# Kernel tuning notes

Measured on AMD Instinct MI355X. Metric: run time of the kernel, lower is better.

Reference implementation:

```python
import jax, jax.numpy as jnp
import numpy as np

B, N, C = 512, 32, 1024


def setup_inputs() -> dict:
    key = jax.random.key(0)
    k1, k2, k3 = jax.random.split(key, 3)
    x = jax.random.normal(k1, (B, N, C), dtype=jnp.float32)
    # Conv1d(in=2, out=1, kernel_size=3): weight [O, I, W], bias [O]
    fan_in = 2 * 3
    bound = 1.0 / np.sqrt(fan_in)
    conv_w = jax.random.uniform(k2, (1, 2, 3), dtype=jnp.float32, minval=-bound, maxval=bound)
    conv_b = jax.random.uniform(k3, (1,), dtype=jnp.float32, minval=-bound, maxval=bound)
    return {"x": x, "conv_w": conv_w, "conv_b": conv_b}


def _merge_step(x, conv_w, conv_b):
    # x: [B, n, C] -> [B, n-1, C]
    b, n, c = x.shape
    # pairwise euclidean distances via gram matrix (avoids [B,n,n,C] blowup)
    sq = jnp.sum(x * x, axis=-1)  # [B, n]
    d2 = sq[:, :, None] + sq[:, None, :] - 2.0 * jnp.einsum('bic,bjc->bij', x, x)
    dist = jnp.sqrt(jnp.maximum(d2, 0.0))  # [B, n, n]
    # global max over ALL batches (as torch.max(all_dist)), then mask diagonal
    m = jnp.max(dist)
    di = jnp.arange(n)
    dist = dist.at[:, di, di].set(m + 1.0)
    # per-batch argmin over flattened matrix, unravel
    flat_idx = jnp.argmin(dist.reshape(b, -1), axis=1)
    a = flat_idx // n
    bb = flat_idx % n
    a, bb = jnp.minimum(a, bb), jnp.maximum(a, bb)  # ensure a < b
    # replicate the exact (buggy-faithful) index-list construction:
    # rows[a]=0; rows[0]=a; rows[b]=1; rows[1]=b  (sequential assignments)
    bi = jnp.arange(b)
    perm = jnp.broadcast_to(jnp.arange(n), (b, n))
    perm = perm.at[bi, a].set(0)
    perm = perm.at[bi, 0].set(a)
    perm = perm.at[bi, bb].set(1)
    perm = perm.at[bi, 1].set(bb)
    xg = jnp.take_along_axis(x, perm[:, :, None], axis=1)  # [B, n, C]
    to_merge = xg[:, 0:2, :]      # [B, 2, C]
    remaining = xg[:, 2:, :]      # [B, n-2, C]
    merged = jax.lax.conv_general_dilated(
        to_merge, conv_w, window_strides=(1,), padding='SAME',
        dimension_numbers=('NCH', 'OIH', 'NCH'))  # [B, 1, C]
    merged = jax.nn.relu(merged + conv_b[None, :, None])
    return jnp.concatenate([merged, remaining], axis=1)


def reference(x, conv_w, conv_b):
    b, n, c = x.shape
    for _ in range(n - 1):
        x = _merge_step(x, conv_w, conv_b)
    return x[:, 0, :]  # final squeeze: [B, C]
```

## Files before the change

kernel.cpp:

```cpp
#include <hip/hip_runtime.h>
#include <stdint.h>

#define BDIM    512
#define NROWS   32
#define CDIM    1024
#define NSTEPS  31
#define BATCH   512

__device__ __forceinline__ float reduce4f(float a0, float a1, float a2, float a3, int lane) {
    float t, r, b01, b23, c;
    t = (lane & 1) ? a0 : a1; r = (lane & 1) ? a1 : a0; b01 = r + __shfl_xor(t, 1);
    t = (lane & 1) ? a2 : a3; r = (lane & 1) ? a3 : a2; b23 = r + __shfl_xor(t, 1);
    t = (lane & 2) ? b01 : b23; r = (lane & 2) ? b23 : b01; c = r + __shfl_xor(t, 2);
    c += __shfl_xor(c, 4); c += __shfl_xor(c, 8); c += __shfl_xor(c, 16); c += __shfl_xor(c, 32);
    return c;
}

__global__ __launch_bounds__(BDIM, 4)
void merge_tree_kernel(const float* __restrict__ xin,
                       const float* __restrict__ wz,
                       const float* __restrict__ bz,
                       float* __restrict__ out)
{
    const int b    = blockIdx.x;
    const int tid  = threadIdx.x;
    const int lane = tid & 63;
    const int wid  = tid >> 6;

    const float* xb = xin + (size_t)b * NROWS * CDIM;

    __shared__ float  D[NROWS][NROWS + 1];
    __shared__ float4 mA4[4 * 64];
    __shared__ float4 mB4[4 * 64];
    __shared__ int    idxbuf[2][NROWS];
    __shared__ int    posb[NROWS];
    __shared__ int    bankSlot[32];
    __shared__ unsigned long long wp[8];

    const float w00 = wz[0], w01 = wz[1], w02 = wz[2];
    const float w10 = wz[3], w11 = wz[4], w12 = wz[5];
    const float cb  = bz[0];

    float R[4][16];
    float m[16];
    float nxt[16];

    if (tid < NROWS) {
        idxbuf[0][tid] = tid;
        posb[tid] = tid;
        bankSlot[tid] = (tid >> 2) + ((tid & 3) << 3);
    }

    {
        const float4* src = (const float4*)xb;
        #pragma unroll
        for (int q = 0; q < 4; q++) {
            float4 t = src[lane * 4 + q];
            m[4*q] = t.x; m[4*q+1] = t.y; m[4*q+2] = t.z; m[4*q+3] = t.w;
        }
    }
    #pragma unroll 1
    for (int i = 0; i < NROWS; i++) {
        if (i < NROWS - 1) {
            const float4* src = (const float4*)(xb + (size_t)(i + 1) * CDIM);
            #pragma unroll
            for (int q = 0; q < 4; q++) {
                float4 t = src[lane * 4 + q];
                nxt[4*q] = t.x; nxt[4*q+1] = t.y; nxt[4*q+2] = t.z; nxt[4*q+3] = t.w;
            }
        }
        float accv[4];
        #pragma unroll
        for (int k = 0; k < 4; k++) {
            const int s = wid + (k << 3);
            float acc0 = 0.0f, acc1 = 0.0f;
            if (s < i) {
                #pragma unroll
                for (int e = 0; e < 8; e++) {
                    float d0 = m[e] - R[k][e];
                    float d1 = m[e + 8] - R[k][e + 8];
                    acc0 += d0 * d0;
                    acc1 += d1 * d1;
                }
            } else if (s == i) {
                #pragma unroll
                for (int e = 0; e < 16; e++) R[k][e] = m[e];
            }
            accv[k] = acc0 + acc1;
        }
        float c = reduce4f(accv[0], accv[1], accv[2], accv[3], lane);
        int s_lane = wid + ((lane & 3) << 3);
        if (lane < 4 && s_lane < i) { D[i][s_lane] = c; D[s_lane][i] = c; }

        if (i < NROWS - 1) {
            #pragma unroll
            for (int e = 0; e < 16; e++) m[e] = nxt[e];
        }
    }
    __syncthreads();

    int p = 0;
    #pragma unroll 1
    for (int step = 0; step < NSTEPS; step++) {
        const int n = NROWS - step;
        int* idx  = idxbuf[p];
        int* nidx = idxbuf[p ^ 1];
        const uint32_t M = 0xFFFFFFFFu / (uint32_t)n + 1u;

        unsigned long long bk = ~0ull;
        #pragma unroll
        for (int r = 0; r < (NROWS * NROWS) / BDIM; r++) {
            const int flat = r * BDIM + tid;
            const int s = flat >> 5, t = flat & 31;
            const int li = posb[s], lj = posb[t];
            if (t > s && li < n && lj < n) {
                uint32_t d2b = __float_as_uint(D[s][t]);
                int i2 = (li < lj) ? li : lj;
                int j2 = (li < lj) ? lj : li;
                unsigned long long key =
                    ((unsigned long long)d2b << 10) | (unsigned)(i2 * n + j2);
                bk = (key < bk) ? key : bk;
            }
        }
        #pragma unroll
        for (int off = 1; off < 64; off <<= 1) {
            unsigned long long ov = __shfl_xor(bk, off);
            bk = (ov < bk) ? ov : bk;
        }
        if (lane == 0) wp[wid] = bk;
        __syncthreads();

        bk = wp[0];
        #pragma unroll
        for (int w = 1; w < 8; w++) {
            unsigned long long ov = wp[w];
            bk = (ov < bk) ? ov : bk;
        }
        const int bp  = (int)(bk & 1023u);
        const int a   = (int)__umulhi((uint32_t)bp, M);
        const int bbj = bp - a * n;
        const int sa  = idx[a], sb = idx[bbj];
        const int deadSlot = (a == 1) ? idx[0] : sa;

        #pragma unroll
        for (int k = 0; k < 4; k++) {
            const int s = bankSlot[wid * 4 + k];
            if (s == sa || s == sb) {
                float hl = __shfl_up(R[k][15], 1);  if (lane == 0)  hl = 0.0f;
                float hr = __shfl_down(R[k][0], 1); if (lane == 63) hr = 0.0f;
                float4* dst = (s == sa) ? mA4 : mB4;
                const float c0 = (s == sa) ? w00 : w10;
                const float c1 = (s == sa) ? w01 : w11;
                const float c2 = (s == sa) ? w02 : w12;
                #pragma unroll
                for (int q = 0; q < 4; q++) {
                    float vv[4];
                    #pragma unroll
                    for (int j = 0; j < 4; j++) {
                        const int e = 4 * q + j;
                        float xm1 = (e == 0)  ? hl : R[k][e - 1];
                        float xp1 = (e == 15) ? hr : R[k][e + 1];
                        vv[j] = c0 * xm1 + c1 * R[k][e] + c2 * xp1;
                    }
                    dst[q * 64 + lane] = make_float4(vv[0], vv[1], vv[2], vv[3]);
                }
            }
        }
        if (tid == 0) { nidx[0] = sb; posb[sb] = 0; posb[deadSlot] = 127; }
        if (tid >= 1 && tid < n - 1) {
            int kk = tid + 1;
            int src = (kk == bbj) ? 1 : ((kk == a) ? 0 : kk);
            int sl2 = idx[src];
            nidx[tid] = sl2;
            posb[sl2] = tid;
        }
        __syncthreads();

        #pragma unroll
        for (int q = 0; q < 4; q++) {
            float4 va = mA4[q * 64 + lane];
            float4 vb = mB4[q * 64 + lane];
            float v0 = cb + va.x + vb.x;
            float v1 = cb + va.y + vb.y;
            float v2 = cb + va.z + vb.z;
            float v3 = cb + va.w + vb.w;
            m[4*q+0] = v0 > 0.0f ? v0 : 0.0f;
            m[4*q+1] = v1 > 0.0f ? v1 : 0.0f;
            m[4*q+2] = v2 > 0.0f ? v2 : 0.0f;
            m[4*q+3] = v3 > 0.0f ? v3 : 0.0f;
        }
        float accv[4]; int slv[4];
        #pragma unroll
        for (int k = 0; k < 4; k++) {
            int s = bankSlot[wid * 4 + k];
            if (s == sb) {
                #pragma unroll
                for (int e = 0; e < 16; e++) R[k][e] = m[e];
            }
            if (s == deadSlot) {
                if (lane == 0) bankSlot[wid * 4 + k] = -1;
                s = -1;
            }
            const int live = (s >= 0 && s != sb) ? s : -1;
            slv[k] = live;
            float acc0 = 0.0f, acc1 = 0.0f;
            if (live >= 0) {
                #pragma unroll
                for (int e = 0; e < 8; e++) {
                    float d0 = m[e] - R[k][e];
                    float d1 = m[e + 8] - R[k][e + 8];
                    acc0 += d0 * d0;
                    acc1 += d1 * d1;
                }
            }
            accv[k] = acc0 + acc1;
        }
        float c = reduce4f(accv[0], accv[1], accv[2], accv[3], lane);
        int s_lane = slv[0];
        s_lane = ((lane & 3) == 1) ? slv[1] : s_lane;
        s_lane = ((lane & 3) == 2) ? slv[2] : s_lane;
        s_lane = ((lane & 3) == 3) ? slv[3] : s_lane;
        if (lane < 4 && s_lane >= 0) {
            D[sb][s_lane] = c; D[s_lane][sb] = c;
        }
        __syncthreads();
        p ^= 1;
    }

    if (wid == 0) {
        float4* od = (float4*)(out + (size_t)b * CDIM);
        #pragma unroll
        for (int q = 0; q < 4; q++)
            od[lane * 4 + q] = make_float4(m[4*q], m[4*q+1], m[4*q+2], m[4*q+3]);
    }
}

extern "C" void kernel_launch(void* const* d_in, const int* in_sizes, int n_in,
                              void* d_out, int out_size, void* d_ws, size_t ws_size,
                              hipStream_t stream) {
    const float* x  = (const float*)d_in[0];
    const float* w  = (const float*)d_in[1];
    const float* cb = (const float*)d_in[2];
    float* out = (float*)d_out;
    (void)d_ws; (void)ws_size; (void)in_sizes; (void)n_in; (void)out_size;

    hipLaunchKernelGGL(merge_tree_kernel, dim3(BATCH), dim3(BDIM), 0, stream,
                       x, w, cb, out);
}
```

Measured before the change: 214.0 us.

## Drop per-step barrier by double-buffering positions and folding new-row distances into argmin

Position lookups are double-buffered and computed directly from the previous permutation, so the per-thread index update no longer scatters into a shared array. The distances of the freshly merged row are reduced per wave into extra partial-min slots, and that row is excluded from the full-matrix scan. This removes the trailing __syncthreads of each merge step. It relies on the remaining barrier to order D writes and wp slot reuse, and on the position encoding (flat index = new position of the partner row, assuming the merged row sits at position 0), which is subtle and could break argmin tie-breaking or introduce races.

Result: slower. 226.5 us (+5.8%).

```diff
diff --git a/kernel.cpp b/kernel.cpp
--- a/kernel.cpp
+++ b/kernel.cpp
@@ -33,9 +33,9 @@
     __shared__ float4 mA4[4 * 64];
     __shared__ float4 mB4[4 * 64];
     __shared__ int    idxbuf[2][NROWS];
-    __shared__ int    posb[NROWS];
+    __shared__ int    posbuf[2][NROWS];
     __shared__ int    bankSlot[32];
-    __shared__ unsigned long long wp[8];
+    __shared__ unsigned long long wp[16];
 
     const float w00 = wz[0], w01 = wz[1], w02 = wz[2];
     const float w10 = wz[3], w11 = wz[4], w12 = wz[5];
@@ -47,9 +47,10 @@
 
     if (tid < NROWS) {
         idxbuf[0][tid] = tid;
-        posb[tid] = tid;
+        posbuf[0][tid] = tid;
         bankSlot[tid] = (tid >> 2) + ((tid & 3) << 3);
     }
+    if (tid < 16) wp[tid] = ~0ull;
 
     {
         const float4* src = (const float4*)xb;
@@ -100,11 +101,14 @@
     __syncthreads();
 
     int p = 0;
+    int sbPrev = 127;
     #pragma unroll 1
     for (int step = 0; step < NSTEPS; step++) {
         const int n = NROWS - step;
         int* idx  = idxbuf[p];
         int* nidx = idxbuf[p ^ 1];
+        int* pos  = posbuf[p];
+        int* npos = posbuf[p ^ 1];
         const uint32_t M = 0xFFFFFFFFu / (uint32_t)n + 1u;
 
         unsigned long long bk = ~0ull;
@@ -112,8 +116,8 @@
         for (int r = 0; r < (NROWS * NROWS) / BDIM; r++) {
             const int flat = r * BDIM + tid;
             const int s = flat >> 5, t = flat & 31;
-            const int li = posb[s], lj = posb[t];
-            if (t > s && li < n && lj < n) {
+            const int li = pos[s], lj = pos[t];
+            if (t > s && li < n && lj < n && s != sbPrev && t != sbPrev) {
                 uint32_t d2b = __float_as_uint(D[s][t]);
                 int i2 = (li < lj) ? li : lj;
                 int j2 = (li < lj) ? lj : li;
@@ -132,7 +136,7 @@
 
         bk = wp[0];
         #pragma unroll
-        for (int w = 1; w < 8; w++) {
+        for (int w = 1; w < 16; w++) {
             unsigned long long ov = wp[w];
             bk = (ov < bk) ? ov : bk;
         }
@@ -166,13 +170,22 @@
                 }
             }
         }
-        if (tid == 0) { nidx[0] = sb; posb[sb] = 0; posb[deadSlot] = 127; }
+        if (tid == 0) nidx[0] = sb;
         if (tid >= 1 && tid < n - 1) {
             int kk = tid + 1;
             int src = (kk == bbj) ? 1 : ((kk == a) ? 0 : kk);
-            int sl2 = idx[src];
-            nidx[tid] = sl2;
-            posb[sl2] = tid;
+            nidx[tid] = idx[src];
+        }
+        if (tid < NROWS) {
+            const int oldp = pos[tid];
+            int np;
+            if (tid == sb)            np = 0;
+            else if (tid == deadSlot) np = 127;
+            else if (oldp >= n)       np = 127;
+            else if (oldp == 0)       np = a - 1;
+            else if (oldp == 1)       np = bbj - 1;
+            else                      np = oldp - 1;
+            npos[tid] = np;
         }
         __syncthreads();
 
@@ -220,10 +233,18 @@
         s_lane = ((lane & 3) == 1) ? slv[1] : s_lane;
         s_lane = ((lane & 3) == 2) ? slv[2] : s_lane;
         s_lane = ((lane & 3) == 3) ? slv[3] : s_lane;
+        unsigned long long nk = ~0ull;
         if (lane < 4 && s_lane >= 0) {
             D[sb][s_lane] = c; D[s_lane][sb] = c;
-        }
-        __syncthreads();
+            const int fl = npos[s_lane];
+            nk = ((unsigned long long)__float_as_uint(c) << 10) | (unsigned)fl;
+        }
+        {
+            unsigned long long ov = __shfl_xor(nk, 1); nk = (ov < nk) ? ov : nk;
+            ov = __shfl_xor(nk, 2);                    nk = (ov < nk) ? ov : nk;
+        }
+        if (lane == 0) wp[8 + wid] = nk;
+        sbPrev = sb;
         p ^= 1;
     }
 
```
